# Kernel tuning notes

Hardware: AMD Instinct MI355X
Metric: run time of the kernel (lower is better)

The kernel has to match this reference:

```python
import jax, jax.numpy as jnp
import numpy as np

N = 50000      # nodes
E = 800000     # edges (avg degree 16)
F_IN = 128     # num_features
H = 64         # hidden_dim
G = 64         # graphs in batch


def setup_inputs() -> dict:
    key = jax.random.key(0)
    ks = jax.random.split(key, 20)
    inp = {
        "x": jax.random.normal(ks[0], (N, F_IN), jnp.float32),
        "edge_index": jax.random.randint(ks[1], (2, E), 0, N, dtype=jnp.int32).astype(jnp.int64),
        "batch": jnp.sort(jax.random.randint(ks[2], (N,), 0, G, dtype=jnp.int32)).astype(jnp.int64),
    }
    # GraphConv layer dims: in -> out
    dims = [(F_IN, H), (H, 2 * H), (2 * H, 3 * H), (3 * H, H)]
    k = 3
    for i, (din, dout) in enumerate(dims):
        s = 1.0 / np.sqrt(din).astype(np.float32)
        inp[f"w{i+1}_rel"] = jax.random.normal(ks[k], (din, dout), jnp.float32) * s
        inp[f"w{i+1}_root"] = jax.random.normal(ks[k + 1], (din, dout), jnp.float32) * s
        inp[f"b{i+1}"] = jnp.zeros((dout,), jnp.float32)
        k += 2
    inp["head_w"] = jax.random.normal(ks[k], (H, 1), jnp.float32) * (1.0 / np.sqrt(H).astype(np.float32))
    inp["head_b"] = jnp.zeros((1,), jnp.float32)
    return inp


def _graph_conv(x, src, dst, w_rel, w_root, b):
    # PyG GraphConv: out = lin_rel(sum_{j in N(i)} x_j) + lin_root(x_i)
    agg = jax.ops.segment_sum(x[src], dst, num_segments=N)  # [N, din]
    return agg @ w_rel + b + x @ w_root


def reference(x, edge_index, batch,
              w1_rel, w1_root, b1,
              w2_rel, w2_root, b2,
              w3_rel, w3_root, b3,
              w4_rel, w4_root, b4,
              head_w, head_b):
    src, dst = edge_index[0], edge_index[1]
    h = jax.nn.relu(_graph_conv(x, src, dst, w1_rel, w1_root, b1))
    h = jax.nn.relu(_graph_conv(h, src, dst, w2_rel, w2_root, b2))
    h = jax.nn.relu(_graph_conv(h, src, dst, w3_rel, w3_root, b3))
    h = _graph_conv(h, src, dst, w4_rel, w4_root, b4)          # [N, H]
    # global_mean_pool over graph ids
    sums = jax.ops.segment_sum(h, batch, num_segments=G)       # [G, H]
    counts = jax.ops.segment_sum(jnp.ones((N,), h.dtype), batch, num_segments=G)
    pooled = sums / jnp.maximum(counts, 1.0)[:, None]          # [G, H]
    return pooled @ head_w + head_b                            # [G, 1]
```

## Files before the change

### kernel.cpp

```cpp
#include <hip/hip_runtime.h>


#define NNODES 50000
#define NEDGES 800000
#define NGRAPH 64
#define NBUK 256
#define BSZ 196
#define EPB (NEDGES / NBUK)
#define CVT_NB (NNODES * 128 / 4 / 256)
#define PACK_NB (160 * 512 / 256)
#define RGRID ((NNODES + 127) / 128)
#define RCHUNK ((RGRID + 7) / 8)

typedef __attribute__((ext_vector_type(8))) __bf16 bf16x8;
typedef __attribute__((ext_vector_type(16))) float f32x16;

__device__ __forceinline__ unsigned short f2bf(float f) {
    unsigned u = __float_as_uint(f);
    u += 0x7fff + ((u >> 16) & 1);
    return (unsigned short)(u >> 16);
}
__device__ __forceinline__ float bf2f(unsigned b) {
    return __uint_as_float(b << 16);
}


__global__ void hist_kernel(const int* __restrict__ dst, int* __restrict__ cnt) {
    __shared__ int h[NBUK];
    int tid = threadIdx.x, k = blockIdx.x;
    h[tid] = 0;
    __syncthreads();
    int end = (k + 1) * EPB;
    for (int i = k * EPB + tid; i < end; i += 256)
        atomicAdd(&h[dst[i] / BSZ], 1);
    __syncthreads();
    cnt[tid * NBUK + k] = h[tid];
}

__global__ void scan1_kernel(int* __restrict__ a, int* __restrict__ bsum, int n) {
    __shared__ int buf[256];
    int tid = threadIdx.x;
    int i = blockIdx.x * 256 + tid;
    int v = (i < n) ? a[i] : 0;
    buf[tid] = v;
    __syncthreads();
    #pragma unroll
    for (int off = 1; off < 256; off <<= 1) {
        int t = (tid >= off) ? buf[tid - off] : 0;
        __syncthreads();
        buf[tid] += t;
        __syncthreads();
    }
    if (i < n) a[i] = buf[tid] - v;
    if (tid == 255) bsum[blockIdx.x] = buf[255];
}

__global__ void scan2_kernel(int* __restrict__ bsum, int nb) {
    __shared__ int buf[256];
    int tid = threadIdx.x;
    int v = (tid < nb) ? bsum[tid] : 0;
    buf[tid] = v;
    __syncthreads();
    #pragma unroll
    for (int off = 1; off < 256; off <<= 1) {
        int t = (tid >= off) ? buf[tid - off] : 0;
        __syncthreads();
        buf[tid] += t;
        __syncthreads();
    }
    if (tid < nb) bsum[tid] = buf[tid] - v;
}

__global__ void scan3_kernel(int* __restrict__ a, const int* __restrict__ bsum, int n) {
    int i = blockIdx.x * 256 + threadIdx.x;
    if (i < n) a[i] += bsum[blockIdx.x];
}

__global__ void partition_kernel(const int* __restrict__ src, const int* __restrict__ dst,
                                 const int* __restrict__ cnt,
                                 unsigned long long* __restrict__ pedge) {
    __shared__ int lbase[NBUK];
    int tid = threadIdx.x, k = blockIdx.x;
    lbase[tid] = cnt[tid * NBUK + k];
    __syncthreads();
    int end = (k + 1) * EPB;
    for (int i = k * EPB + tid; i < end; i += 256) {
        int s = src[i], d = dst[i];
        int pos = atomicAdd(&lbase[d / BSZ], 1);
        pedge[pos] = (unsigned long long)(unsigned)s | ((unsigned long long)(unsigned)d << 32);
    }
}

__global__ void build_kernel(const unsigned long long* __restrict__ pedge,
                             const int* __restrict__ cnt,
                             int* __restrict__ rp, int* __restrict__ csr) {
    __shared__ int sdeg[256], sc[256], sbase[256], sfill[256];
    int tid = threadIdx.x, b = blockIdx.x;
    int node0 = b * BSZ;
    int ncnt = NNODES - node0;
    if (ncnt > BSZ) ncnt = BSZ;
    if (ncnt < 0) ncnt = 0;
    int seg0 = cnt[b * NBUK];
    int seg1 = (b + 1 < NBUK) ? cnt[(b + 1) * NBUK] : NEDGES;
    sdeg[tid] = 0;
    sfill[tid] = 0;
    __syncthreads();
    for (int i = seg0 + tid; i < seg1; i += 256)
        atomicAdd(&sdeg[(int)(pedge[i] >> 32) - node0], 1);
    __syncthreads();
    sc[tid] = sdeg[tid];
    __syncthreads();
    #pragma unroll
    for (int off = 1; off < 256; off <<= 1) {
        int t = (tid >= off) ? sc[tid - off] : 0;
        __syncthreads();
        sc[tid] += t;
        __syncthreads();
    }
    sbase[tid] = sc[tid] - sdeg[tid];
    if (tid < ncnt) rp[node0 + tid] = seg0 + sbase[tid];
    if (b == NBUK - 1 && tid == 0) rp[NNODES] = NEDGES;
    __syncthreads();
    for (int i = seg0 + tid; i < seg1; i += 256) {
        unsigned long long p = pedge[i];
        int d = (int)(p >> 32) - node0;
        int pos = atomicAdd(&sfill[d], 1);
        csr[seg0 + sbase[d] + pos] = (int)(p & 0xffffffffu);
    }
}


__device__ __forceinline__ void pack32(const float* __restrict__ W, unsigned short* __restrict__ dst,
                                       int KS_tot, int ks0, int dcols, int ct0,
                                       int tl, int ksl, int lane, int j) {
    int k = ksl * 16 + ((lane >> 5) << 3) + j;
    int col = tl * 32 + (lane & 31);
    dst[(((size_t)(ct0 + tl) * KS_tot + (ks0 + ksl)) * 64 + lane) * 8 + j] = f2bf(W[k * dcols + col]);
}

__global__ void prep_kernel(const float* __restrict__ x, unsigned short* __restrict__ xbf,
                            const float* __restrict__ w1_rel, const float* __restrict__ w1_root,
                            const float* __restrict__ w2_rel, const float* __restrict__ w2_root,
                            const float* __restrict__ w3_rel, const float* __restrict__ w3_root,
                            unsigned short* __restrict__ pL1, unsigned short* __restrict__ pL2,
                            unsigned short* __restrict__ pL3,
                            const float* __restrict__ w4_rel, const float* __restrict__ w4_root,
                            const float* __restrict__ b4, const float* __restrict__ head_w,
                            float* __restrict__ wr, float* __restrict__ wt,
                            float* __restrict__ cbuf) {
    int b = blockIdx.x;
    int tid = threadIdx.x;
    if (b < CVT_NB) {
        int i = b * 256 + tid;
        float4 v = ((const float4*)x)[i];
        unsigned lo = (unsigned)f2bf(v.x) | ((unsigned)f2bf(v.y) << 16);
        unsigned hi = (unsigned)f2bf(v.z) | ((unsigned)f2bf(v.w) << 16);
        ((uint2*)xbf)[i] = make_uint2(lo, hi);
    } else if (b < CVT_NB + PACK_NB) {
        int idx = (b - CVT_NB) * 256 + tid;
        int g = idx >> 9;
        int t = idx & 511;
        int lane = (t >> 3) & 63, j = t & 7;
        if (g < 16)       { int gl = g;       pack32(w1_rel,  pL1, 8,  0, 64,  0, gl / 8, gl % 8, lane, j); }
        else if (g < 32)  { int gl = g - 16;  pack32(w1_root, pL1, 8,  0, 64,  2, gl / 8, gl % 8, lane, j); }
        else if (g < 48)  { int gl = g - 32;  pack32(w2_rel,  pL2, 8,  0, 128, 0, gl / 4, gl % 4, lane, j); }
        else if (g < 64)  { int gl = g - 48;  pack32(w2_root, pL2, 8,  4, 128, 0, gl / 4, gl % 4, lane, j); }
        else if (g < 112) { int gl = g - 64;  pack32(w3_rel,  pL3, 16, 0, 192, 0, gl / 8, gl % 8, lane, j); }
        else              { int gl = g - 112; pack32(w3_root, pL3, 16, 8, 192, 0, gl / 8, gl % 8, lane, j); }
    } else {
        if (tid < 192) {
            float ar = 0.f, at = 0.f;
            for (int j = 0; j < 64; j++) {
                float hw = head_w[j];
                ar = fmaf(w4_rel[tid * 64 + j], hw, ar);
                at = fmaf(w4_root[tid * 64 + j], hw, at);
            }
            wr[tid] = ar;
            wt[tid] = at;
        } else if (tid == 192) {
            float c = 0.f;
            for (int j = 0; j < 64; j++) c = fmaf(b4[j], head_w[j], c);
            cbuf[0] = c;
        }
    }
}


template<int KS, int NC>
__global__ __launch_bounds__(256, 4) void gemm_v4(
    const unsigned short* __restrict__ A, const unsigned short* __restrict__ W,
    const float* __restrict__ bias, unsigned short* __restrict__ OUT,
    int ldo, int ocol0, int relu, int N)
{
    const int K = KS * 16;
    int i = blockIdx.x;
    int chunk = i / (NC * 8);
    int rem = i - chunk * (NC * 8);
    int cg = rem >> 3;
    int rowb = chunk * 8 + (rem & 7);
    int tid = threadIdx.x;
    int wave = tid >> 6, lane = tid & 63;
    int l32 = lane & 31, half = lane >> 5;
    int rbase = rowb * 128 + wave * 32;
    if (rbase >= N) return;

    int arow = rbase + l32;
    if (arow >= N) arow = N - 1;
    const unsigned short* ap = A + (size_t)arow * K + half * 8;
    const unsigned short* wp = W + (size_t)cg * KS * 512 + lane * 8;

    f32x16 acc;
    #pragma unroll
    for (int r = 0; r < 16; r++) acc[r] = 0.f;

    #pragma unroll 1
    for (int kb = 0; kb < KS; kb += 8) {
        bf16x8 areg[8], breg[8];
        #pragma unroll
        for (int j = 0; j < 8; j++) {
            areg[j] = *(const bf16x8*)(ap + (kb + j) * 16);
            breg[j] = *(const bf16x8*)(wp + (size_t)(kb + j) * 512);
        }
        #pragma unroll
        for (int j = 0; j < 8; j++)
            acc = __builtin_amdgcn_mfma_f32_32x32x16_bf16(areg[j], breg[j], acc, 0, 0, 0);
    }

    int col = cg * 32 + l32;
    float bi = bias ? bias[col] : 0.f;
    #pragma unroll
    for (int reg = 0; reg < 16; reg++) {
        int row = rbase + (reg & 3) + 8 * (reg >> 2) + 4 * half;
        if (row < N) {
            float v = acc[reg] + bi;
            if (relu) v = fmaxf(v, 0.f);
            OUT[(size_t)row * ldo + ocol0 + col] = f2bf(v);
        }
    }
}


__device__ __forceinline__ void acc8(float* a, uint4 u) {
    a[0] += bf2f(u.x & 0xffffu); a[1] += bf2f(u.x >> 16);
    a[2] += bf2f(u.y & 0xffffu); a[3] += bf2f(u.y >> 16);
    a[4] += bf2f(u.z & 0xffffu); a[5] += bf2f(u.z >> 16);
    a[6] += bf2f(u.w & 0xffffu); a[7] += bf2f(u.w >> 16);
}

template<int LPF>
__global__ void agg_kernel_v2(const unsigned short* __restrict__ X, int ldx,
                              const int* __restrict__ rp, const int* __restrict__ csr,
                              const unsigned short* __restrict__ root, int ldr,
                              const float* __restrict__ bias, int relu,
                              unsigned short* __restrict__ OUT, int ldo, int N) {
    int t = blockIdx.x * blockDim.x + threadIdx.x;
    int node = t / (2 * LPF);
    int r = t % (2 * LPF);
    int sub = r / LPF;
    int sl = r % LPF;
    if (node >= N) return;
    float a[8] = {0.f, 0.f, 0.f, 0.f, 0.f, 0.f, 0.f, 0.f};
    int e0 = rp[node], e1 = rp[node + 1];
    const unsigned short* xb = X + 8 * sl;
    int e = e0 + sub;
    for (; e + 2 < e1; e += 4) {
        int s0 = csr[e], s1 = csr[e + 2];
        uint4 u0 = *(const uint4*)(xb + (size_t)s0 * ldx);
        uint4 u1 = *(const uint4*)(xb + (size_t)s1 * ldx);
        acc8(a, u0);
        acc8(a, u1);
    }
    if (e < e1) {
        uint4 u = *(const uint4*)(xb + (size_t)csr[e] * ldx);
        acc8(a, u);
    }
    #pragma unroll
    for (int i = 0; i < 8; i++) a[i] += __shfl_xor(a[i], LPF, 64);
    if (sub == 0) {
        if (root) {
            uint4 u = *(const uint4*)(root + (size_t)node * ldr + 8 * sl);
            acc8(a, u);
        }
        if (bias) {
            float4 b0 = *(const float4*)(bias + 8 * sl);
            float4 b1 = *(const float4*)(bias + 8 * sl + 4);
            a[0] += b0.x; a[1] += b0.y; a[2] += b0.z; a[3] += b0.w;
            a[4] += b1.x; a[5] += b1.y; a[6] += b1.z; a[7] += b1.w;
        }
        if (relu) {
            #pragma unroll
            for (int i = 0; i < 8; i++) a[i] = fmaxf(a[i], 0.f);
        }
        uint4 o;
        o.x = (unsigned)f2bf(a[0]) | ((unsigned)f2bf(a[1]) << 16);
        o.y = (unsigned)f2bf(a[2]) | ((unsigned)f2bf(a[3]) << 16);
        o.z = (unsigned)f2bf(a[4]) | ((unsigned)f2bf(a[5]) << 16);
        o.w = (unsigned)f2bf(a[6]) | ((unsigned)f2bf(a[7]) << 16);
        *(uint4*)(OUT + (size_t)node * ldo + 8 * sl) = o;
    }
}


__global__ void st_kernel(const unsigned short* __restrict__ h3, const float* __restrict__ wr,
                          const float* __restrict__ wt, float* __restrict__ s,
                          float* __restrict__ t, int N) {
    int lane = threadIdx.x & 63;
    int node = (blockIdx.x * blockDim.x + threadIdx.x) >> 6;
    if (node >= N) return;
    float as = 0.f, at = 0.f;
    if (lane < 48) {
        uint2 u = *(const uint2*)(h3 + (size_t)node * 192 + 4 * lane);
        float x0 = bf2f(u.x & 0xffffu), x1 = bf2f(u.x >> 16);
        float x2 = bf2f(u.y & 0xffffu), x3 = bf2f(u.y >> 16);
        float4 r4 = *(const float4*)(wr + 4 * lane);
        float4 t4 = *(const float4*)(wt + 4 * lane);
        as = x0 * r4.x + x1 * r4.y + x2 * r4.z + x3 * r4.w;
        at = x0 * t4.x + x1 * t4.y + x2 * t4.z + x3 * t4.w;
    }
    #pragma unroll
    for (int off = 32; off > 0; off >>= 1) {
        as += __shfl_down(as, off, 64);
        at += __shfl_down(at, off, 64);
    }
    if (lane == 0) { s[node] = as; t[node] = at; }
}

__global__ void aggpool_kernel(const float* __restrict__ s, const float* __restrict__ t,
                               const int* __restrict__ rp, const int* __restrict__ csr,
                               const int* __restrict__ batch, float* __restrict__ gsum,
                               int* __restrict__ cnt, int N) {
    __shared__ float ls[NGRAPH];
    __shared__ int lc[NGRAPH];
    int tid = threadIdx.x;
    if (tid < NGRAPH) { ls[tid] = 0.f; lc[tid] = 0; }
    __syncthreads();
    int n = blockIdx.x * blockDim.x + tid;
    if (n < N) {
        float a = 0.f;
        int e = rp[n], e1 = rp[n + 1];
        for (; e + 3 < e1; e += 4) {
            int s0 = csr[e], s1 = csr[e + 1], s2 = csr[e + 2], s3 = csr[e + 3];
            a += s[s0] + s[s1] + s[s2] + s[s3];
        }
        for (; e < e1; e++) a += s[csr[e]];
        int g = batch[n];
        atomicAdd(&ls[g], a + t[n]);
        atomicAdd(&lc[g], 1);
    }
    __syncthreads();
    if (tid < NGRAPH && lc[tid] > 0) {
        atomicAdd(&gsum[tid], ls[tid]);
        atomicAdd(&cnt[tid], lc[tid]);
    }
}

__global__ void final_kernel(const float* __restrict__ gsum, const int* __restrict__ cnt,
                             const float* __restrict__ cbuf, const float* __restrict__ head_b,
                             float* __restrict__ out) {
    int g = threadIdx.x;
    if (g < NGRAPH) {
        float c = (float)(cnt[g] > 0 ? cnt[g] : 1);
        out[g] = gsum[g] / c + cbuf[0] + head_b[0];
    }
}


extern "C" void kernel_launch(void* const* d_in, const int* in_sizes, int n_in,
                              void* d_out, int out_size, void* d_ws, size_t ws_size,
                              hipStream_t stream) {
    const float* x       = (const float*)d_in[0];
    const int*   edge    = (const int*)d_in[1];
    const int*   batch   = (const int*)d_in[2];
    const float* w1_rel  = (const float*)d_in[3];
    const float* w1_root = (const float*)d_in[4];
    const float* b1      = (const float*)d_in[5];
    const float* w2_rel  = (const float*)d_in[6];
    const float* w2_root = (const float*)d_in[7];
    const float* b2      = (const float*)d_in[8];
    const float* w3_rel  = (const float*)d_in[9];
    const float* w3_root = (const float*)d_in[10];
    const float* b3      = (const float*)d_in[11];
    const float* w4_rel  = (const float*)d_in[12];
    const float* w4_root = (const float*)d_in[13];
    const float* b4      = (const float*)d_in[14];
    const float* head_w  = (const float*)d_in[15];
    const float* head_b  = (const float*)d_in[16];
    float* out = (float*)d_out;

    const int N = NNODES, E = NEDGES;
    const int* src = edge;
    const int* dst = edge + E;

    char* ws = (char*)d_ws;
    size_t off = 0;
    auto alloc = [&](size_t bytes) -> char* {
        char* p = ws + off;
        off = (off + bytes + 255) & ~(size_t)255;
        return p;
    };
    float* gsum  = (float*)alloc(NGRAPH * 4);
    int*   cnt   = (int*)alloc(NGRAPH * 4);
    size_t zero_bytes = off;
    int*   bcnt  = (int*)alloc((size_t)NBUK * NBUK * 4);
    int*   bsum  = (int*)alloc(256 * 4);
    int*   rp    = (int*)alloc((size_t)(N + 1) * 4);
    int*   csr   = (int*)alloc((size_t)E * 4);
    unsigned long long* pedge = (unsigned long long*)alloc((size_t)E * 8);
    unsigned short* xbf    = (unsigned short*)alloc((size_t)N * 128 * 2);
    unsigned short* z1     = (unsigned short*)alloc((size_t)N * 128 * 2);
    unsigned short* combo2 = (unsigned short*)alloc((size_t)N * 128 * 2);
    unsigned short* combo3 = (unsigned short*)alloc((size_t)N * 256 * 2);
    unsigned short* h3     = (unsigned short*)alloc((size_t)N * 192 * 2);
    unsigned short* pL1    = (unsigned short*)alloc(4 * 8 * 512 * 2);
    unsigned short* pL2    = (unsigned short*)alloc(4 * 8 * 512 * 2);
    unsigned short* pL3    = (unsigned short*)alloc(6 * 16 * 512 * 2);
    float* sbuf  = (float*)alloc((size_t)N * 4);
    float* tbuf  = (float*)alloc((size_t)N * 4);
    float* wr    = (float*)alloc(192 * 4);
    float* wt    = (float*)alloc(192 * 4);
    float* cbuf  = (float*)alloc(4);
    (void)ws_size;

    hipMemsetAsync(gsum, 0, zero_bytes, stream);

    const int TB = 256;

    hist_kernel<<<NBUK, 256, 0, stream>>>(dst, bcnt);
    scan1_kernel<<<NBUK, 256, 0, stream>>>(bcnt, bsum, NBUK * NBUK);
    scan2_kernel<<<1, 256, 0, stream>>>(bsum, NBUK);
    scan3_kernel<<<NBUK, 256, 0, stream>>>(bcnt, bsum, NBUK * NBUK);
    partition_kernel<<<NBUK, 256, 0, stream>>>(src, dst, bcnt, pedge);
    build_kernel<<<NBUK, 256, 0, stream>>>(pedge, bcnt, rp, csr);

    prep_kernel<<<CVT_NB + PACK_NB + 1, 256, 0, stream>>>(
        x, xbf, w1_rel, w1_root, w2_rel, w2_root, w3_rel, w3_root,
        pL1, pL2, pL3, w4_rel, w4_root, b4, head_w, wr, wt, cbuf);

    gemm_v4<8, 4><<<RCHUNK * 8 * 4, 256, 0, stream>>>(xbf, pL1, nullptr, z1, 128, 0, 0, N);
    agg_kernel_v2<8><<<(N * 16 + TB - 1) / TB, TB, 0, stream>>>(z1, 128, rp, csr,
                                                                z1 + 64, 128, b1, 1, combo2 + 64, 128, N);
    agg_kernel_v2<8><<<(N * 16 + TB - 1) / TB, TB, 0, stream>>>(combo2 + 64, 128, rp, csr,
                                                                nullptr, 0, nullptr, 0, combo2, 128, N);
    gemm_v4<8, 4><<<RCHUNK * 8 * 4, 256, 0, stream>>>(combo2, pL2, b2, combo3, 256, 128, 1, N);
    agg_kernel_v2<16><<<(N * 32 + TB - 1) / TB, TB, 0, stream>>>(combo3 + 128, 256, rp, csr,
                                                                 nullptr, 0, nullptr, 0, combo3, 256, N);
    gemm_v4<16, 6><<<RCHUNK * 8 * 6, 256, 0, stream>>>(combo3, pL3, b3, h3, 192, 0, 1, N);

    st_kernel<<<(N * 64 + TB - 1) / TB, TB, 0, stream>>>(h3, wr, wt, sbuf, tbuf, N);
    aggpool_kernel<<<(N + TB - 1) / TB, TB, 0, stream>>>(sbuf, tbuf, rp, csr, batch, gsum, cnt, N);
    final_kernel<<<1, 64, 0, stream>>>(gsum, cnt, cbuf, head_b, out);
}
```

Baseline: 276.7 us.

## Widen edge splitting in aggregation, fold scan3 and final kernel, add sched barrier

The aggregation kernels now split each node's edge list across 4 sub-groups instead of 2 and combine them with xor shuffles. The pooling aggregation also uses 4 lanes per node. The scan3 fixup kernel is removed by adding the block offset inside partition and build. The final kernel is folded into aggpool through a last-block-done counter. A sched_barrier is placed between loads and MFMAs in the GEMM. Together these aim to raise memory-level parallelism on gathers and cut launch count, at the cost of more shuffles and more idle lanes on low-degree nodes.

```diff
diff --git a/kernel.cpp b/kernel.cpp
--- a/kernel.cpp
+++ b/kernel.cpp
@@ -71,17 +71,12 @@
     if (tid < nb) bsum[tid] = buf[tid] - v;
 }
 
-__global__ void scan3_kernel(int* __restrict__ a, const int* __restrict__ bsum, int n) {
-    int i = blockIdx.x * 256 + threadIdx.x;
-    if (i < n) a[i] += bsum[blockIdx.x];
-}
-
 __global__ void partition_kernel(const int* __restrict__ src, const int* __restrict__ dst,
-                                 const int* __restrict__ cnt,
+                                 const int* __restrict__ cnt, const int* __restrict__ bsum,
                                  unsigned long long* __restrict__ pedge) {
     __shared__ int lbase[NBUK];
     int tid = threadIdx.x, k = blockIdx.x;
-    lbase[tid] = cnt[tid * NBUK + k];
+    lbase[tid] = cnt[tid * NBUK + k] + bsum[tid];
     __syncthreads();
     int end = (k + 1) * EPB;
     for (int i = k * EPB + tid; i < end; i += 256) {
@@ -92,7 +87,7 @@
 }
 
 __global__ void build_kernel(const unsigned long long* __restrict__ pedge,
-                             const int* __restrict__ cnt,
+                             const int* __restrict__ bsum,
                              int* __restrict__ rp, int* __restrict__ csr) {
     __shared__ int sdeg[256], sc[256], sbase[256], sfill[256];
     int tid = threadIdx.x, b = blockIdx.x;
@@ -100,8 +95,8 @@
     int ncnt = NNODES - node0;
     if (ncnt > BSZ) ncnt = BSZ;
     if (ncnt < 0) ncnt = 0;
-    int seg0 = cnt[b * NBUK];
-    int seg1 = (b + 1 < NBUK) ? cnt[(b + 1) * NBUK] : NEDGES;
+    int seg0 = bsum[b];
+    int seg1 = (b + 1 < NBUK) ? bsum[b + 1] : NEDGES;
     sdeg[tid] = 0;
     sfill[tid] = 0;
     __syncthreads();
@@ -221,6 +216,7 @@
             areg[j] = *(const bf16x8*)(ap + (kb + j) * 16);
             breg[j] = *(const bf16x8*)(wp + (size_t)(kb + j) * 512);
         }
+        __builtin_amdgcn_sched_barrier(0);
         #pragma unroll
         for (int j = 0; j < 8; j++)
             acc = __builtin_amdgcn_mfma_f32_32x32x16_bf16(areg[j], breg[j], acc, 0, 0, 0);
@@ -247,15 +243,15 @@
     a[6] += bf2f(u.w & 0xffffu); a[7] += bf2f(u.w >> 16);
 }
 
-template<int LPF>
-__global__ void agg_kernel_v2(const unsigned short* __restrict__ X, int ldx,
+template<int LPF, int SUBS>
+__global__ void agg_kernel_v3(const unsigned short* __restrict__ X, int ldx,
                               const int* __restrict__ rp, const int* __restrict__ csr,
                               const unsigned short* __restrict__ root, int ldr,
                               const float* __restrict__ bias, int relu,
                               unsigned short* __restrict__ OUT, int ldo, int N) {
     int t = blockIdx.x * blockDim.x + threadIdx.x;
-    int node = t / (2 * LPF);
-    int r = t % (2 * LPF);
+    int node = t / (SUBS * LPF);
+    int r = t % (SUBS * LPF);
     int sub = r / LPF;
     int sl = r % LPF;
     if (node >= N) return;
@@ -263,8 +259,8 @@
     int e0 = rp[node], e1 = rp[node + 1];
     const unsigned short* xb = X + 8 * sl;
     int e = e0 + sub;
-    for (; e + 2 < e1; e += 4) {
-        int s0 = csr[e], s1 = csr[e + 2];
+    for (; e + SUBS < e1; e += 2 * SUBS) {
+        int s0 = csr[e], s1 = csr[e + SUBS];
         uint4 u0 = *(const uint4*)(xb + (size_t)s0 * ldx);
         uint4 u1 = *(const uint4*)(xb + (size_t)s1 * ldx);
         acc8(a, u0);
@@ -275,7 +271,9 @@
         acc8(a, u);
     }
     #pragma unroll
-    for (int i = 0; i < 8; i++) a[i] += __shfl_xor(a[i], LPF, 64);
+    for (int m = LPF; m < SUBS * LPF; m <<= 1)
+        #pragma unroll
+        for (int i = 0; i < 8; i++) a[i] += __shfl_xor(a[i], m, 64);
     if (sub == 0) {
         if (root) {
             uint4 u = *(const uint4*)(root + (size_t)node * ldr + 8 * sl);
@@ -328,39 +326,48 @@
 __global__ void aggpool_kernel(const float* __restrict__ s, const float* __restrict__ t,
                                const int* __restrict__ rp, const int* __restrict__ csr,
                                const int* __restrict__ batch, float* __restrict__ gsum,
-                               int* __restrict__ cnt, int N) {
+                               int* __restrict__ cnt, int* __restrict__ done,
+                               const float* __restrict__ cbuf, const float* __restrict__ head_b,
+                               float* __restrict__ out, int N) {
     __shared__ float ls[NGRAPH];
     __shared__ int lc[NGRAPH];
+    __shared__ int lastflag;
     int tid = threadIdx.x;
     if (tid < NGRAPH) { ls[tid] = 0.f; lc[tid] = 0; }
     __syncthreads();
-    int n = blockIdx.x * blockDim.x + tid;
-    if (n < N) {
+    int gidx = blockIdx.x * blockDim.x + tid;
+    int node = gidx >> 2, sub = gidx & 3;
+    if (node < N) {
         float a = 0.f;
-        int e = rp[n], e1 = rp[n + 1];
-        for (; e + 3 < e1; e += 4) {
-            int s0 = csr[e], s1 = csr[e + 1], s2 = csr[e + 2], s3 = csr[e + 3];
-            a += s[s0] + s[s1] + s[s2] + s[s3];
-        }
-        for (; e < e1; e++) a += s[csr[e]];
-        int g = batch[n];
-        atomicAdd(&ls[g], a + t[n]);
-        atomicAdd(&lc[g], 1);
+        int e = rp[node] + sub, e1 = rp[node + 1];
+        for (; e + 4 < e1; e += 8) a += s[csr[e]] + s[csr[e + 4]];
+        if (e < e1) a += s[csr[e]];
+        a += __shfl_xor(a, 1, 64);
+        a += __shfl_xor(a, 2, 64);
+        if (sub == 0) {
+            int g = batch[node];
+            atomicAdd(&ls[g], a + t[node]);
+            atomicAdd(&lc[g], 1);
+        }
     }
     __syncthreads();
     if (tid < NGRAPH && lc[tid] > 0) {
         atomicAdd(&gsum[tid], ls[tid]);
         atomicAdd(&cnt[tid], lc[tid]);
     }
-}
-
-__global__ void final_kernel(const float* __restrict__ gsum, const int* __restrict__ cnt,
-                             const float* __restrict__ cbuf, const float* __restrict__ head_b,
-                             float* __restrict__ out) {
-    int g = threadIdx.x;
-    if (g < NGRAPH) {
-        float c = (float)(cnt[g] > 0 ? cnt[g] : 1);
-        out[g] = gsum[g] / c + cbuf[0] + head_b[0];
+    __syncthreads();
+    if (tid == 0) {
+        __threadfence();
+        int d = atomicAdd(done, 1);
+        lastflag = (d == (int)gridDim.x - 1);
+    }
+    __syncthreads();
+    if (lastflag && tid < NGRAPH) {
+        __threadfence();
+        float gs = atomicAdd(&gsum[tid], 0.0f);
+        int c = atomicAdd(&cnt[tid], 0);
+        float cc = (float)(c > 0 ? c : 1);
+        out[tid] = gs / cc + cbuf[0] + head_b[0];
     }
 }
 
@@ -400,6 +407,7 @@
     };
     float* gsum  = (float*)alloc(NGRAPH * 4);
     int*   cnt   = (int*)alloc(NGRAPH * 4);
+    int*   done  = (int*)alloc(4);
     size_t zero_bytes = off;
     int*   bcnt  = (int*)alloc((size_t)NBUK * NBUK * 4);
     int*   bsum  = (int*)alloc(256 * 4);
@@ -428,25 +436,24 @@
     hist_kernel<<<NBUK, 256, 0, stream>>>(dst, bcnt);
     scan1_kernel<<<NBUK, 256, 0, stream>>>(bcnt, bsum, NBUK * NBUK);
     scan2_kernel<<<1, 256, 0, stream>>>(bsum, NBUK);
-    scan3_kernel<<<NBUK, 256, 0, stream>>>(bcnt, bsum, NBUK * NBUK);
-    partition_kernel<<<NBUK, 256, 0, stream>>>(src, dst, bcnt, pedge);
-    build_kernel<<<NBUK, 256, 0, stream>>>(pedge, bcnt, rp, csr);
+    partition_kernel<<<NBUK, 256, 0, stream>>>(src, dst, bcnt, bsum, pedge);
+    build_kernel<<<NBUK, 256, 0, stream>>>(pedge, bsum, rp, csr);
 
     prep_kernel<<<CVT_NB + PACK_NB + 1, 256, 0, stream>>>(
         x, xbf, w1_rel, w1_root, w2_rel, w2_root, w3_rel, w3_root,
         pL1, pL2, pL3, w4_rel, w4_root, b4, head_w, wr, wt, cbuf);
 
     gemm_v4<8, 4><<<RCHUNK * 8 * 4, 256, 0, stream>>>(xbf, pL1, nullptr, z1, 128, 0, 0, N);
-    agg_kernel_v2<8><<<(N * 16 + TB - 1) / TB, TB, 0, stream>>>(z1, 128, rp, csr,
-                                                                z1 + 64, 128, b1, 1, combo2 + 64, 128, N);
-    agg_kernel_v2<8><<<(N * 16 + TB - 1) / TB, TB, 0, stream>>>(combo2 + 64, 128, rp, csr,
-                                                                nullptr, 0, nullptr, 0, combo2, 128, N);
+    agg_kernel_v3<8, 4><<<(N * 32 + TB - 1) / TB, TB, 0, stream>>>(z1, 128, rp, csr,
+                                                                   z1 + 64, 128, b1, 1, combo2 + 64, 128, N);
+    agg_kernel_v3<8, 4><<<(N * 32 + TB - 1) / TB, TB, 0, stream>>>(combo2 + 64, 128, rp, csr,
+                                                                   nullptr, 0, nullptr, 0, combo2, 128, N);
     gemm_v4<8, 4><<<RCHUNK * 8 * 4, 256, 0, stream>>>(combo2, pL2, b2, combo3, 256, 128, 1, N);
-    agg_kernel_v2<16><<<(N * 32 + TB - 1) / TB, TB, 0, stream>>>(combo3 + 128, 256, rp, csr,
-                                                                 nullptr, 0, nullptr, 0, combo3, 256, N);
+    agg_kernel_v3<16, 4><<<(N * 64 + TB - 1) / TB, TB, 0, stream>>>(combo3 + 128, 256, rp, csr,
+                                                                    nullptr, 0, nullptr, 0, combo3, 256, N);
     gemm_v4<16, 6><<<RCHUNK * 8 * 6, 256, 0, stream>>>(combo3, pL3, b3, h3, 192, 0, 1, N);
 
     st_kernel<<<(N * 64 + TB - 1) / TB, TB, 0, stream>>>(h3, wr, wt, sbuf, tbuf, N);
-    aggpool_kernel<<<(N + TB - 1) / TB, TB, 0, stream>>>(sbuf, tbuf, rp, csr, batch, gsum, cnt, N);
-    final_kernel<<<1, 64, 0, stream>>>(gsum, cnt, cbuf, head_b, out);
-}
+    aggpool_kernel<<<(N * 4 + TB - 1) / TB, TB, 0, stream>>>(sbuf, tbuf, rp, csr, batch,
+                                                             gsum, cnt, done, cbuf, head_b, out, N);
+}
```

After: 291.4 us. +5.3%, slower.
